# Kernel optimization log

Measured on AMD Instinct MI355X. Metric: run time of the kernel, lower is better.

Reference implementation:

```python
import jax, jax.numpy as jnp
import numpy as np

NQ = 12          # num_qubits
NL = 5           # num_layers
NA = 4           # num_actions
DIM = 2 ** NQ    # state-vector dimension

# PennyLane convention: wire 0 is the most-significant bit of the state index.
_idx = np.arange(DIM)
_bits = (_idx[:, None] >> (NQ - 1 - np.arange(NQ))) & 1           # [DIM, NQ]
_cz = np.ones(DIM)
for _i in range(NQ):                                              # ring of CZs (all diagonal -> fuse)
    _cz *= np.where((_bits[:, _i] & _bits[:, (_i + 1) % NQ]) == 1, -1.0, 1.0)
CZ_RING = jnp.asarray(_cz, dtype=jnp.complex64)                   # [DIM]
ZTAB = jnp.asarray(1 - 2 * _bits[:, :NA], dtype=jnp.float32)      # [DIM, NA] PauliZ eigenvalues


def _bc(v):
    # broadcast an angle-derived scalar or [B] vector against [B, lead, trail]
    v = jnp.asarray(v)
    return v.reshape(v.shape + (1, 1))


def _apply_1q(state, wire, m00, m01, m10, m11):
    b = state.shape[0]
    lead, trail = 2 ** wire, 2 ** (NQ - 1 - wire)
    s = state.reshape(b, lead, 2, trail)
    s0, s1 = s[:, :, 0, :], s[:, :, 1, :]
    return jnp.stack([m00 * s0 + m01 * s1, m10 * s0 + m11 * s1], axis=2).reshape(b, DIM)


def _rx(state, wire, theta):
    c = _bc(jnp.cos(0.5 * theta)).astype(jnp.complex64)
    s = _bc(jnp.sin(0.5 * theta)).astype(jnp.complex64)
    return _apply_1q(state, wire, c, -1j * s, -1j * s, c)


def _ry(state, wire, theta):
    c = _bc(jnp.cos(0.5 * theta)).astype(jnp.complex64)
    s = _bc(jnp.sin(0.5 * theta)).astype(jnp.complex64)
    return _apply_1q(state, wire, c, -s, s, c)


def _rz(state, wire, theta):
    # diagonal gate: no mixing across the wire axis
    b = state.shape[0]
    lead, trail = 2 ** wire, 2 ** (NQ - 1 - wire)
    e = _bc(jnp.exp(-0.5j * theta))  # e^{-i t/2}; conj(e) = e^{+i t/2} for real t
    s = state.reshape(b, lead, 2, trail)
    return jnp.stack([e * s[:, :, 0, :], jnp.conj(e) * s[:, :, 1, :]], axis=2).reshape(b, DIM)


def setup_inputs() -> dict:
    key = jax.random.key(0)
    k1, k2 = jax.random.split(key)
    x = jax.random.normal(k1, (4096, 4 * NQ), dtype=jnp.float32)
    input_scaling = jnp.ones((NL, 3, NQ), dtype=jnp.float32)
    weights = jax.random.uniform(k2, (NL, 3, 2 * NQ), dtype=jnp.float32,
                                 minval=-np.pi, maxval=np.pi)
    output_scaling = jnp.ones((NA,), dtype=jnp.float32)
    return {"x": x, "input_scaling": input_scaling, "weights": weights,
            "output_scaling": output_scaling}


def reference(x, input_scaling, weights, output_scaling):
    b = x.shape[0]
    feats = (x[:, NQ:2 * NQ], x[:, 2 * NQ:3 * NQ], x[:, 3 * NQ:4 * NQ])
    state = jnp.zeros((b, DIM), dtype=jnp.complex64).at[:, 0].set(1.0)
    for layer in range(NL):
        for blk in range(3):
            f = feats[blk]
            for i in range(NQ):
                state = _rx(state, i, input_scaling[layer, blk, i] * f[:, i])
            for i in range(NQ):
                state = _ry(state, i, weights[layer, blk, i])
            for i in range(NQ):
                state = _rz(state, i, weights[layer, blk, i + NQ])
            state = state * CZ_RING[None, :]
    probs = state.real ** 2 + state.imag ** 2          # [B, DIM]
    expvals = probs @ ZTAB                             # [B, NA] <Z_i>
    return expvals * output_scaling                    # logits
```

## Files before the change

kernel.cpp:

```cpp
#include <hip/hip_runtime.h>
#include <stdint.h>

#define NQ 12
#define NL 5
#define AMPS 16


typedef float f2 __attribute__((ext_vector_type(2)));

static __device__ __forceinline__ float f_u(unsigned u) { return __uint_as_float(u); }
static __device__ __forceinline__ unsigned u_f(float f) { return __float_as_uint(f); }

#define PK_MUL_RR(acc, C, S) \
    asm("v_pk_mul_f32 %0, %1, %2 op_sel_hi:[0,1]" : "=v"(acc) : "v"(C), "v"(S))
#define PK_FMA_I(acc, C, S) \
    asm("v_pk_fma_f32 %0, %1, %2, %0 op_sel:[1,1,0] op_sel_hi:[1,0,1] neg_lo:[1,0,0]" \
        : "+v"(acc) : "v"(C), "v"(S))
#define PK_FMA_R(acc, C, S) \
    asm("v_pk_fma_f32 %0, %1, %2, %0 op_sel_hi:[0,1,1]" : "+v"(acc) : "v"(C), "v"(S))
#define PK_FMA_IC(acc, C, S) \
    asm("v_pk_fma_f32 %0, %1, %2, %0 op_sel:[1,1,0] op_sel_hi:[1,0,1] neg_hi:[1,0,0]" \
        : "+v"(acc) : "v"(C), "v"(S))
#define PK_FMA_RN(acc, C, S) \
    asm("v_pk_fma_f32 %0, %1, %2, %0 op_sel_hi:[0,1,1] neg_lo:[1,0,0] neg_hi:[1,0,0]" \
        : "+v"(acc) : "v"(C), "v"(S))

#define CPLX_AB(DST, CA, S, CB, O)                                    \
    { f2 t_;                                                          \
      PK_MUL_RR(t_, CA, S); PK_FMA_I(t_, CA, S);                      \
      PK_FMA_R (t_, CB, O); PK_FMA_I(t_, CB, O);                      \
      DST = t_; }

template <int CTRL>
static __device__ __forceinline__ float dpp_xor(float v) {
    int u = (int)__float_as_uint(v);
    return __uint_as_float((unsigned)__builtin_amdgcn_update_dpp(u, u, CTRL, 0xF, 0xF, false));
}
static __device__ __forceinline__ float swz_xor4(float v) {
    return f_u((unsigned)__builtin_amdgcn_ds_swizzle((int)u_f(v), 0x101F));
}

#define COEF(Q)                                                         \
    const float ar_ = f_u(__builtin_amdgcn_readlane(u_f(ar), (Q)));     \
    const float ai_ = f_u(__builtin_amdgcn_readlane(u_f(ai), (Q)));     \
    const float br_ = f_u(__builtin_amdgcn_readlane(u_f(br), (Q)));     \
    const float bi_ = f_u(__builtin_amdgcn_readlane(u_f(bi), (Q)));

#define AB_GATE_PK(OPX)                                                 \
    _Pragma("unroll")                                                   \
    for (int r = 0; r < AMPS; ++r) {                                    \
        f2 o; o.x = OPX(s[r].x); o.y = OPX(s[r].y);                     \
        CPLX_AB(s[r], CA, s[r], CB, o)                                  \
    }

template <int ST>
static __device__ __forceinline__ void reg_gate_pk(f2 (&s)[AMPS], f2 CAg, f2 CBg) {
#pragma unroll
    for (int r0 = 0; r0 < AMPS; ++r0) {
        if (r0 & ST) continue;
        const int r1 = r0 | ST;
        const f2 s0 = s[r0], s1 = s[r1];
        f2 t0, t1;
        PK_MUL_RR(t0, CAg, s0); PK_FMA_I (t0, CAg, s0);
        PK_FMA_R (t0, CBg, s1); PK_FMA_I (t0, CBg, s1);
        PK_MUL_RR(t1, CAg, s1); PK_FMA_IC(t1, CAg, s1);
        PK_FMA_RN(t1, CBg, s0); PK_FMA_I (t1, CBg, s0);
        s[r0] = t0; s[r1] = t1;
    }
}

__global__ __launch_bounds__(256)
void qsim_kernel(
    const float* __restrict__ x,
    const float* __restrict__ iscale,
    const float* __restrict__ w,
    const float* __restrict__ oscale,
    float* __restrict__ out,
    int batch)
{
    const int tid  = threadIdx.x;
    const int lane = tid & 63;
    const int wv   = tid >> 6;
    const int b    = blockIdx.x;
    if (b >= batch) return;

    __shared__ float4 xch[8 * 256];

    f2 s[AMPS];
#pragma unroll
    for (int r = 0; r < AMPS; ++r) { s[r].x = 0.f; s[r].y = 0.f; }
    if (tid == 0) s[0].x = 1.f;

    unsigned czm = 0;
#pragma unroll
    for (int r = 0; r < AMPS; ++r) {
        unsigned idx  = ((unsigned)wv << 10) | ((unsigned)lane << 4) | (unsigned)r;
        unsigned adj  = (idx & (idx >> 1)) & 0x7FFu;
        unsigned wrap = (idx & (idx >> 11)) & 1u;
        czm |= (((unsigned)__popc(adj) + wrap) & 1u) << r;
    }

    const int ql = (lane < NQ) ? lane : 0;
    const float* xb = x + (size_t)b * (4 * NQ);

#pragma unroll 1
    for (int it = 0; it < NL * 3; ++it) {
        const int blk = it - 3 * (it / 3);

        float f     = xb[NQ + blk * NQ + ql];
        float alpha = iscale[it * NQ + ql] * f;
        float beta  = w[it * 2 * NQ + ql];
        float gamma = w[it * 2 * NQ + NQ + ql];
        float sa, ca, sb, cb, sg, cg;
        sincosf(0.5f * alpha, &sa, &ca);
        sincosf(0.5f * beta,  &sb, &cb);
        sincosf(0.5f * gamma, &sg, &cg);
        float cbca = cb * ca, sbsa = sb * sa, sbca = sb * ca, cbsa = cb * sa;
        float ar =  cg * cbca + sg * sbsa;
        float ai =  cg * sbsa - sg * cbca;
        float br = -(cg * sbca + sg * cbsa);
        float bi =  sg * sbca - cg * cbsa;

        {
            COEF(0);
            const int bit = (wv >> 1) & 1;
            const f2 CA = { ar_, bit ? -ai_ : ai_ };
            const f2 CB = { bit ? -br_ : br_, bi_ };
            __syncthreads();
#pragma unroll
            for (int k = 0; k < 8; ++k)
                xch[(k << 8) + tid] = make_float4(s[2*k].x, s[2*k].y, s[2*k+1].x, s[2*k+1].y);
            __syncthreads();
            const int ptid = tid ^ (2 << 6);
#pragma unroll
            for (int k = 0; k < 8; ++k) {
                float4 o4 = xch[(k << 8) + ptid];
                f2 oA = { o4.x, o4.y }, oB = { o4.z, o4.w };
                CPLX_AB(s[2*k],   CA, s[2*k],   CB, oA)
                CPLX_AB(s[2*k+1], CA, s[2*k+1], CB, oB)
            }
        }
        {
            COEF(1);
            const int bit = wv & 1;
            const f2 CA = { ar_, bit ? -ai_ : ai_ };
            const f2 CB = { bit ? -br_ : br_, bi_ };
            __syncthreads();
#pragma unroll
            for (int k = 0; k < 8; ++k)
                xch[(k << 8) + tid] = make_float4(s[2*k].x, s[2*k].y, s[2*k+1].x, s[2*k+1].y);
            __syncthreads();
            const int ptid = tid ^ (1 << 6);
#pragma unroll
            for (int k = 0; k < 8; ++k) {
                float4 o4 = xch[(k << 8) + ptid];
                f2 oA = { o4.x, o4.y }, oB = { o4.z, o4.w };
                CPLX_AB(s[2*k],   CA, s[2*k],   CB, oA)
                CPLX_AB(s[2*k+1], CA, s[2*k+1], CB, oB)
            }
        }

        {
            COEF(2);
            const int hb = (lane >> 5) & 1;
            const f2 CP = { hb ? -br_ : ar_, hb ?  bi_ : ai_ };
            const f2 CQ = { hb ?  ar_ : br_, hb ? -ai_ : bi_ };
#pragma unroll
            for (int r = 0; r < AMPS; ++r) {
                auto dx = __builtin_amdgcn_permlane32_swap(u_f(s[r].x), u_f(s[r].x), false, false);
                auto dy = __builtin_amdgcn_permlane32_swap(u_f(s[r].y), u_f(s[r].y), false, false);
                f2 na = { f_u(dx[0]), f_u(dy[0]) };
                f2 nb = { f_u(dx[1]), f_u(dy[1]) };
                CPLX_AB(s[r], CP, na, CQ, nb)
            }
        }
        {
            COEF(3);
            const int hb = (lane >> 4) & 1;
            const f2 CP = { hb ? -br_ : ar_, hb ?  bi_ : ai_ };
            const f2 CQ = { hb ?  ar_ : br_, hb ? -ai_ : bi_ };
#pragma unroll
            for (int r = 0; r < AMPS; ++r) {
                auto dx = __builtin_amdgcn_permlane16_swap(u_f(s[r].x), u_f(s[r].x), false, false);
                auto dy = __builtin_amdgcn_permlane16_swap(u_f(s[r].y), u_f(s[r].y), false, false);
                f2 na = { f_u(dx[0]), f_u(dy[0]) };
                f2 nb = { f_u(dx[1]), f_u(dy[1]) };
                CPLX_AB(s[r], CP, na, CQ, nb)
            }
        }
        {
            COEF(4);
            const int bit = (lane >> 3) & 1;
            const f2 CA = { ar_, bit ? -ai_ : ai_ };
            const f2 CB = { bit ? -br_ : br_, bi_ };
            AB_GATE_PK(dpp_xor<0x128>)
        }
        {
            COEF(5);
            const int bit = (lane >> 2) & 1;
            const f2 CA = { ar_, bit ? -ai_ : ai_ };
            const f2 CB = { bit ? -br_ : br_, bi_ };
            AB_GATE_PK(swz_xor4)
        }
        {
            COEF(6);
            const int bit = (lane >> 1) & 1;
            const f2 CA = { ar_, bit ? -ai_ : ai_ };
            const f2 CB = { bit ? -br_ : br_, bi_ };
            AB_GATE_PK(dpp_xor<0x4E>)
        }
        {
            COEF(7);
            const int bit = lane & 1;
            const f2 CA = { ar_, bit ? -ai_ : ai_ };
            const f2 CB = { bit ? -br_ : br_, bi_ };
            AB_GATE_PK(dpp_xor<0xB1>)
        }

        { COEF(8);  const f2 CAg = { ar_, ai_ }, CBg = { br_, bi_ }; reg_gate_pk<8>(s, CAg, CBg); }
        { COEF(9);  const f2 CAg = { ar_, ai_ }, CBg = { br_, bi_ }; reg_gate_pk<4>(s, CAg, CBg); }
        { COEF(10); const f2 CAg = { ar_, ai_ }, CBg = { br_, bi_ }; reg_gate_pk<2>(s, CAg, CBg); }
        { COEF(11); const f2 CAg = { ar_, ai_ }, CBg = { br_, bi_ }; reg_gate_pk<1>(s, CAg, CBg); }

#pragma unroll
        for (int r = 0; r < AMPS; ++r) {
            const unsigned sgn = ((czm >> r) & 1u) << 31;
            s[r].x = f_u(u_f(s[r].x) ^ sgn);
            s[r].y = f_u(u_f(s[r].y) ^ sgn);
        }
    }

    float p = 0.f;
#pragma unroll
    for (int r = 0; r < AMPS; ++r) p = fmaf(s[r].x, s[r].x, fmaf(s[r].y, s[r].y, p));

    float v0 = ((wv   >> 1) & 1) ? -p : p;
    float v1 = ( wv         & 1) ? -p : p;
    float v2 = ((lane >> 5) & 1) ? -p : p;
    float v3 = ((lane >> 4) & 1) ? -p : p;
#pragma unroll
    for (int m = 1; m <= 32; m <<= 1) {
        v0 += __shfl_xor(v0, m);
        v1 += __shfl_xor(v1, m);
        v2 += __shfl_xor(v2, m);
        v3 += __shfl_xor(v3, m);
    }

    __syncthreads();
    if (lane == 0) xch[wv] = make_float4(v0, v1, v2, v3);
    __syncthreads();
    if (tid == 0) {
        float4 a0 = xch[0], a1 = xch[1], a2 = xch[2], a3 = xch[3];
        float4 o;
        o.x = (a0.x + a1.x + a2.x + a3.x) * oscale[0];
        o.y = (a0.y + a1.y + a2.y + a3.y) * oscale[1];
        o.z = (a0.z + a1.z + a2.z + a3.z) * oscale[2];
        o.w = (a0.w + a1.w + a2.w + a3.w) * oscale[3];
        *reinterpret_cast<float4*>(out + (size_t)b * 4) = o;
    }
}

extern "C" void kernel_launch(void* const* d_in, const int* in_sizes, int n_in,
                              void* d_out, int out_size, void* d_ws, size_t ws_size,
                              hipStream_t stream) {
    const float* x      = (const float*)d_in[0];
    const float* iscale = (const float*)d_in[1];
    const float* w      = (const float*)d_in[2];
    const float* oscale = (const float*)d_in[3];
    float* out          = (float*)d_out;

    const int batch = in_sizes[0] / (4 * NQ);
    qsim_kernel<<<batch, 256, 0, stream>>>(x, iscale, w, oscale, out, batch);
}
```

Baseline: 610.4 us.

## Fuse cross-wave qubit gates into one LDS exchange and precompute gate coefficients

Qubits 0 and 1, which span waves, are now combined into a single 4x4 tensor-product gate. This needs one LDS write/read round with three partner reads instead of two separate exchanges, which halves the barriers and LDS stores per layer. All gate coefficients for every iteration are computed up front by the first 180 threads into shared memory, replacing per-iteration sincos and readlane broadcasts. The gate order within an iteration is also changed so register-local gates run before lane shuffles, and the swizzle gate batches its shuffles. The cost is more FMAs per amplitude for the fused gate, three LDS reads per slot, and more register pressure from holding 12 float4 coefficients.

```diff
diff --git a/kernel.cpp b/kernel.cpp
--- a/kernel.cpp
+++ b/kernel.cpp
@@ -3,6 +3,7 @@
 
 #define NQ 12
 #define NL 5
+#define NIT 15
 #define AMPS 16
 
 
@@ -25,6 +26,9 @@
     asm("v_pk_fma_f32 %0, %1, %2, %0 op_sel_hi:[0,1,1] neg_lo:[1,0,0] neg_hi:[1,0,0]" \
         : "+v"(acc) : "v"(C), "v"(S))
 
+#define CMUL(DST, CA, CB) \
+    { PK_MUL_RR(DST, CA, CB); PK_FMA_I(DST, CA, CB); }
+
 #define CPLX_AB(DST, CA, S, CB, O)                                    \
     { f2 t_;                                                          \
       PK_MUL_RR(t_, CA, S); PK_FMA_I(t_, CA, S);                      \
@@ -39,12 +43,6 @@
 static __device__ __forceinline__ float swz_xor4(float v) {
     return f_u((unsigned)__builtin_amdgcn_ds_swizzle((int)u_f(v), 0x101F));
 }
-
-#define COEF(Q)                                                         \
-    const float ar_ = f_u(__builtin_amdgcn_readlane(u_f(ar), (Q)));     \
-    const float ai_ = f_u(__builtin_amdgcn_readlane(u_f(ai), (Q)));     \
-    const float br_ = f_u(__builtin_amdgcn_readlane(u_f(br), (Q)));     \
-    const float bi_ = f_u(__builtin_amdgcn_readlane(u_f(bi), (Q)));
 
 #define AB_GATE_PK(OPX)                                                 \
     _Pragma("unroll")                                                   \
@@ -82,35 +80,19 @@
     const int lane = tid & 63;
     const int wv   = tid >> 6;
     const int b    = blockIdx.x;
-    if (b >= batch) return;
 
     __shared__ float4 xch[8 * 256];
-
-    f2 s[AMPS];
-#pragma unroll
-    for (int r = 0; r < AMPS; ++r) { s[r].x = 0.f; s[r].y = 0.f; }
-    if (tid == 0) s[0].x = 1.f;
-
-    unsigned czm = 0;
-#pragma unroll
-    for (int r = 0; r < AMPS; ++r) {
-        unsigned idx  = ((unsigned)wv << 10) | ((unsigned)lane << 4) | (unsigned)r;
-        unsigned adj  = (idx & (idx >> 1)) & 0x7FFu;
-        unsigned wrap = (idx & (idx >> 11)) & 1u;
-        czm |= (((unsigned)__popc(adj) + wrap) & 1u) << r;
-    }
-
-    const int ql = (lane < NQ) ? lane : 0;
-    const float* xb = x + (size_t)b * (4 * NQ);
-
-#pragma unroll 1
-    for (int it = 0; it < NL * 3; ++it) {
+    __shared__ float4 coef[NIT * NQ];
+
+    if (tid < NIT * NQ) {
+        const int it  = tid / NQ;
+        const int q   = tid - it * NQ;
         const int blk = it - 3 * (it / 3);
-
-        float f     = xb[NQ + blk * NQ + ql];
-        float alpha = iscale[it * NQ + ql] * f;
-        float beta  = w[it * 2 * NQ + ql];
-        float gamma = w[it * 2 * NQ + NQ + ql];
+        const float* xb = x + (size_t)b * (4 * NQ);
+        float f     = xb[NQ + blk * NQ + q];
+        float alpha = iscale[it * NQ + q] * f;
+        float beta  = w[it * 2 * NQ + q];
+        float gamma = w[it * 2 * NQ + NQ + q];
         float sa, ca, sb, cb, sg, cg;
         sincosf(0.5f * alpha, &sa, &ca);
         sincosf(0.5f * beta,  &sb, &cb);
@@ -120,51 +102,94 @@
         float ai =  cg * sbsa - sg * cbca;
         float br = -(cg * sbca + sg * cbsa);
         float bi =  sg * sbca - cg * cbsa;
-
-        {
-            COEF(0);
-            const int bit = (wv >> 1) & 1;
-            const f2 CA = { ar_, bit ? -ai_ : ai_ };
-            const f2 CB = { bit ? -br_ : br_, bi_ };
+        coef[tid] = make_float4(ar, ai, br, bi);
+    }
+
+    f2 s[AMPS];
+#pragma unroll
+    for (int r = 0; r < AMPS; ++r) { s[r].x = 0.f; s[r].y = 0.f; }
+    if (tid == 0) s[0].x = 1.f;
+
+    unsigned czm = 0;
+#pragma unroll
+    for (int r = 0; r < AMPS; ++r) {
+        unsigned idx  = ((unsigned)wv << 10) | ((unsigned)lane << 4) | (unsigned)r;
+        unsigned adj  = (idx & (idx >> 1)) & 0x7FFu;
+        unsigned wrap = (idx & (idx >> 11)) & 1u;
+        czm |= (((unsigned)__popc(adj) + wrap) & 1u) << r;
+    }
+
+    const unsigned sw1 = (unsigned)((wv >> 1) & 1) << 31;
+    const unsigned sw0 = (unsigned)(wv & 1) << 31;
+    const bool hb2 = (lane >> 5) & 1;
+    const bool hb3 = (lane >> 4) & 1;
+    const unsigned sb4 = (unsigned)((lane >> 3) & 1) << 31;
+    const unsigned sb5 = (unsigned)((lane >> 2) & 1) << 31;
+    const unsigned sb6 = (unsigned)((lane >> 1) & 1) << 31;
+    const unsigned sb7 = (unsigned)(lane & 1) << 31;
+
+    const int t64  = tid ^ 64;
+    const int t128 = tid ^ 128;
+    const int t192 = tid ^ 192;
+
+    __syncthreads();
+
+#pragma unroll 1
+    for (int it = 0; it < NIT; ++it) {
+        float4 c[NQ];
+#pragma unroll
+        for (int q = 0; q < NQ; ++q) c[q] = coef[it * NQ + q];
+
+        {
+            const f2 A0 = { c[0].x, f_u(u_f(c[0].y) ^ sw1) };
+            const f2 B0 = { f_u(u_f(c[0].z) ^ sw1), c[0].w };
+            const f2 A1 = { c[1].x, f_u(u_f(c[1].y) ^ sw0) };
+            const f2 B1 = { f_u(u_f(c[1].z) ^ sw0), c[1].w };
+            f2 Cs, C64, C128, C192;
+            CMUL(Cs,   A0, A1)
+            CMUL(C64,  A0, B1)
+            CMUL(C128, B0, A1)
+            CMUL(C192, B0, B1)
+
             __syncthreads();
 #pragma unroll
             for (int k = 0; k < 8; ++k)
                 xch[(k << 8) + tid] = make_float4(s[2*k].x, s[2*k].y, s[2*k+1].x, s[2*k+1].y);
             __syncthreads();
-            const int ptid = tid ^ (2 << 6);
 #pragma unroll
             for (int k = 0; k < 8; ++k) {
-                float4 o4 = xch[(k << 8) + ptid];
-                f2 oA = { o4.x, o4.y }, oB = { o4.z, o4.w };
-                CPLX_AB(s[2*k],   CA, s[2*k],   CB, oA)
-                CPLX_AB(s[2*k+1], CA, s[2*k+1], CB, oB)
-            }
-        }
-        {
-            COEF(1);
-            const int bit = wv & 1;
-            const f2 CA = { ar_, bit ? -ai_ : ai_ };
-            const f2 CB = { bit ? -br_ : br_, bi_ };
-            __syncthreads();
-#pragma unroll
-            for (int k = 0; k < 8; ++k)
-                xch[(k << 8) + tid] = make_float4(s[2*k].x, s[2*k].y, s[2*k+1].x, s[2*k+1].y);
-            __syncthreads();
-            const int ptid = tid ^ (1 << 6);
-#pragma unroll
-            for (int k = 0; k < 8; ++k) {
-                float4 o4 = xch[(k << 8) + ptid];
-                f2 oA = { o4.x, o4.y }, oB = { o4.z, o4.w };
-                CPLX_AB(s[2*k],   CA, s[2*k],   CB, oA)
-                CPLX_AB(s[2*k+1], CA, s[2*k+1], CB, oB)
-            }
-        }
-
-        {
-            COEF(2);
-            const int hb = (lane >> 5) & 1;
-            const f2 CP = { hb ? -br_ : ar_, hb ?  bi_ : ai_ };
-            const f2 CQ = { hb ?  ar_ : br_, hb ? -ai_ : bi_ };
+                const float4 p1 = xch[(k << 8) + t64];
+                const float4 p2 = xch[(k << 8) + t128];
+                const float4 p3 = xch[(k << 8) + t192];
+                {
+                    const f2 o1 = { p1.x, p1.y }, o2 = { p2.x, p2.y }, o3 = { p3.x, p3.y };
+                    f2 t0;
+                    PK_MUL_RR(t0, Cs, s[2*k]); PK_FMA_I(t0, Cs, s[2*k]);
+                    PK_FMA_R(t0, C64,  o1);    PK_FMA_I(t0, C64,  o1);
+                    PK_FMA_R(t0, C128, o2);    PK_FMA_I(t0, C128, o2);
+                    PK_FMA_R(t0, C192, o3);    PK_FMA_I(t0, C192, o3);
+                    s[2*k] = t0;
+                }
+                {
+                    const f2 o1 = { p1.z, p1.w }, o2 = { p2.z, p2.w }, o3 = { p3.z, p3.w };
+                    f2 t1;
+                    PK_MUL_RR(t1, Cs, s[2*k+1]); PK_FMA_I(t1, Cs, s[2*k+1]);
+                    PK_FMA_R(t1, C64,  o1);      PK_FMA_I(t1, C64,  o1);
+                    PK_FMA_R(t1, C128, o2);      PK_FMA_I(t1, C128, o2);
+                    PK_FMA_R(t1, C192, o3);      PK_FMA_I(t1, C192, o3);
+                    s[2*k+1] = t1;
+                }
+            }
+        }
+
+        { const f2 CA = { c[8].x,  c[8].y  }, CB = { c[8].z,  c[8].w  }; reg_gate_pk<8>(s, CA, CB); }
+        { const f2 CA = { c[9].x,  c[9].y  }, CB = { c[9].z,  c[9].w  }; reg_gate_pk<4>(s, CA, CB); }
+        { const f2 CA = { c[10].x, c[10].y }, CB = { c[10].z, c[10].w }; reg_gate_pk<2>(s, CA, CB); }
+        { const f2 CA = { c[11].x, c[11].y }, CB = { c[11].z, c[11].w }; reg_gate_pk<1>(s, CA, CB); }
+
+        {
+            const f2 CP = { hb2 ? -c[2].z : c[2].x, hb2 ?  c[2].w : c[2].y };
+            const f2 CQ = { hb2 ?  c[2].x : c[2].z, hb2 ? -c[2].y : c[2].w };
 #pragma unroll
             for (int r = 0; r < AMPS; ++r) {
                 auto dx = __builtin_amdgcn_permlane32_swap(u_f(s[r].x), u_f(s[r].x), false, false);
@@ -175,10 +200,8 @@
             }
         }
         {
-            COEF(3);
-            const int hb = (lane >> 4) & 1;
-            const f2 CP = { hb ? -br_ : ar_, hb ?  bi_ : ai_ };
-            const f2 CQ = { hb ?  ar_ : br_, hb ? -ai_ : bi_ };
+            const f2 CP = { hb3 ? -c[3].z : c[3].x, hb3 ?  c[3].w : c[3].y };
+            const f2 CQ = { hb3 ?  c[3].x : c[3].z, hb3 ? -c[3].y : c[3].w };
 #pragma unroll
             for (int r = 0; r < AMPS; ++r) {
                 auto dx = __builtin_amdgcn_permlane16_swap(u_f(s[r].x), u_f(s[r].x), false, false);
@@ -189,38 +212,38 @@
             }
         }
         {
-            COEF(4);
-            const int bit = (lane >> 3) & 1;
-            const f2 CA = { ar_, bit ? -ai_ : ai_ };
-            const f2 CB = { bit ? -br_ : br_, bi_ };
+            const f2 CA = { c[4].x, f_u(u_f(c[4].y) ^ sb4) };
+            const f2 CB = { f_u(u_f(c[4].z) ^ sb4), c[4].w };
             AB_GATE_PK(dpp_xor<0x128>)
         }
         {
-            COEF(5);
-            const int bit = (lane >> 2) & 1;
-            const f2 CA = { ar_, bit ? -ai_ : ai_ };
-            const f2 CB = { bit ? -br_ : br_, bi_ };
-            AB_GATE_PK(swz_xor4)
-        }
-        {
-            COEF(6);
-            const int bit = (lane >> 1) & 1;
-            const f2 CA = { ar_, bit ? -ai_ : ai_ };
-            const f2 CB = { bit ? -br_ : br_, bi_ };
+            const f2 CA = { c[5].x, f_u(u_f(c[5].y) ^ sb5) };
+            const f2 CB = { f_u(u_f(c[5].z) ^ sb5), c[5].w };
+#pragma unroll
+            for (int h = 0; h < 2; ++h) {
+                float ox[8], oy[8];
+#pragma unroll
+                for (int r = 0; r < 8; ++r) {
+                    ox[r] = swz_xor4(s[h*8 + r].x);
+                    oy[r] = swz_xor4(s[h*8 + r].y);
+                }
+#pragma unroll
+                for (int r = 0; r < 8; ++r) {
+                    f2 o = { ox[r], oy[r] };
+                    CPLX_AB(s[h*8 + r], CA, s[h*8 + r], CB, o)
+                }
+            }
+        }
+        {
+            const f2 CA = { c[6].x, f_u(u_f(c[6].y) ^ sb6) };
+            const f2 CB = { f_u(u_f(c[6].z) ^ sb6), c[6].w };
             AB_GATE_PK(dpp_xor<0x4E>)
         }
         {
-            COEF(7);
-            const int bit = lane & 1;
-            const f2 CA = { ar_, bit ? -ai_ : ai_ };
-            const f2 CB = { bit ? -br_ : br_, bi_ };
+            const f2 CA = { c[7].x, f_u(u_f(c[7].y) ^ sb7) };
+            const f2 CB = { f_u(u_f(c[7].z) ^ sb7), c[7].w };
             AB_GATE_PK(dpp_xor<0xB1>)
         }
-
-        { COEF(8);  const f2 CAg = { ar_, ai_ }, CBg = { br_, bi_ }; reg_gate_pk<8>(s, CAg, CBg); }
-        { COEF(9);  const f2 CAg = { ar_, ai_ }, CBg = { br_, bi_ }; reg_gate_pk<4>(s, CAg, CBg); }
-        { COEF(10); const f2 CAg = { ar_, ai_ }, CBg = { br_, bi_ }; reg_gate_pk<2>(s, CAg, CBg); }
-        { COEF(11); const f2 CAg = { ar_, ai_ }, CBg = { br_, bi_ }; reg_gate_pk<1>(s, CAg, CBg); }
 
 #pragma unroll
         for (int r = 0; r < AMPS; ++r) {
```

After: 537.4 us. 1.14x faster.
